# Kernel optimization log

Measured on AMD Instinct MI355X. Metric: run time of the kernel, lower is better.

The kernel has to match this reference:

```python
import jax, jax.numpy as jnp
import numpy as np

N_NODES = 50000
N_EDGES = 800000
IN_DIM = 128
OUT_DIM = 128
NUM_RELS = 8


def setup_inputs() -> dict:
    key = jax.random.key(0)
    k_feat, k_rel, k_w, k_src, k_dst, k_rt = jax.random.split(key, 6)
    feat = jax.random.normal(k_feat, (N_NODES, IN_DIM), dtype=jnp.float32)
    # xavier_uniform over (in_dim, out_dim) fan
    limit = float(np.sqrt(6.0 / (IN_DIM + OUT_DIM)))
    rel_emb = jax.random.uniform(k_rel, (NUM_RELS, IN_DIM, OUT_DIM), dtype=jnp.float32,
                                 minval=-limit, maxval=limit)
    edge_weight = jax.random.uniform(k_w, (N_EDGES,), dtype=jnp.float32)
    src = jax.random.randint(k_src, (N_EDGES,), 0, N_NODES, dtype=jnp.int32)
    dst = jax.random.randint(k_dst, (N_EDGES,), 0, N_NODES, dtype=jnp.int32)
    rel_type = jax.random.randint(k_rt, (N_EDGES,), 0, NUM_RELS, dtype=jnp.int32)
    return {"feat": feat, "rel_emb": rel_emb, "edge_weight": edge_weight,
            "src": src, "dst": dst, "rel_type": rel_type}


def reference(feat, rel_emb, edge_weight, src, dst, rel_type):
    # src_feat: [E, in] gather of source-node features
    src_feat = feat[src]
    num_rels = rel_emb.shape[0]
    # Equivalent to bmm(src_feat[:,None,:], rel_emb[rel_type]).squeeze(1)
    # but avoids materializing the [E, in, out] per-edge weight tensor:
    # loop over the small fixed relation set with masked accumulation.
    msg = jnp.zeros((src_feat.shape[0], rel_emb.shape[2]), dtype=src_feat.dtype)
    for r in range(num_rels):
        mask = (rel_type == r)[:, None]
        msg = msg + jnp.where(mask, src_feat @ rel_emb[r], jnp.zeros((), dtype=src_feat.dtype))
    msg = msg * edge_weight[:, None]
    # copy_e + sum aggregation onto destination nodes: [N, out]
    return jax.ops.segment_sum(msg, dst, num_segments=feat.shape[0])
```

## Files before the change

kernel.cpp:

```cpp
#include <hip/hip_runtime.h>
#include <stdint.h>

#define N_NODES   50000
#define N_EDGES   800000
#define IN_DIM    128
#define OUT_DIM   128
#define NUM_RELS  8
#define THREADS   256

typedef _Float16 half_t;
typedef _Float16 half2v __attribute__((ext_vector_type(2)));
typedef _Float16 half4v __attribute__((ext_vector_type(4)));
typedef _Float16 half8 __attribute__((ext_vector_type(8)));
typedef float floatx4 __attribute__((ext_vector_type(4)));


#define NBINS3    N_NODES
#define NB3       ((NBINS3 + 1023) / 1024)

#define WS_Y2     0
#define WS_OFF    102400000
#define WS_WT     102600064
#define WS_BASE   102862208
#define WS_WGT    106062208
#define WS_HIST   107662208
#define WS_BSUM   107862208
#define WS_NEED   (size_t)107862464

__global__ void prep_hist_kernel(const float* __restrict__ rel_emb, half_t* __restrict__ WT,
                                 const int* __restrict__ dst, int* __restrict__ hist) {
    int b = blockIdx.x;
    if (b < 512) {
        int t = b * 256 + threadIdx.x;
        int r = t >> 14, k = (t >> 7) & 127, n = t & 127;
        WT[(size_t)((r << 7) | n) * 128 + k] = (half_t)rel_emb[t];
    } else {
        int i = (b - 512) * 256 + threadIdx.x;
        if (i < N_EDGES) atomicAdd(&hist[dst[i]], 1);
    }
}

__global__ void scan1_kernel(const int* __restrict__ hist, int* __restrict__ bsum) {
    __shared__ int sh[256];
    int b = blockIdx.x, t = threadIdx.x;
    int i0 = b * 1024 + t * 4;
    int s = 0;
    #pragma unroll
    for (int j = 0; j < 4; j++) { int idx = i0 + j; if (idx < NBINS3) s += hist[idx]; }
    sh[t] = s; __syncthreads();
    for (int o = 128; o > 0; o >>= 1) { if (t < o) sh[t] += sh[t + o]; __syncthreads(); }
    if (t == 0) bsum[b] = sh[0];
}

__global__ void scan2_kernel(int* __restrict__ bsum, int* __restrict__ off) {
    __shared__ int sh[64];
    int t = threadIdx.x;
    int v = (t < NB3) ? bsum[t] : 0;
    sh[t] = v; __syncthreads();
    for (int o = 1; o < 64; o <<= 1) {
        int x = (t >= o) ? sh[t - o] : 0;
        __syncthreads();
        sh[t] += x;
        __syncthreads();
    }
    if (t < NB3) bsum[t] = sh[t] - v;
    if (t == 0) off[NBINS3] = N_EDGES;
}

__global__ void scan3_kernel(const int* __restrict__ hist, const int* __restrict__ boff,
                             int* __restrict__ off, int* __restrict__ cursors) {
    __shared__ int sh[256];
    int b = blockIdx.x, t = threadIdx.x;
    int i0 = b * 1024 + t * 4;
    int v[4]; int s = 0;
    #pragma unroll
    for (int j = 0; j < 4; j++) { int idx = i0 + j; v[j] = (idx < NBINS3) ? hist[idx] : 0; s += v[j]; }
    sh[t] = s; __syncthreads();
    for (int o = 1; o < 256; o <<= 1) {
        int x = (t >= o) ? sh[t - o] : 0;
        __syncthreads();
        sh[t] += x;
        __syncthreads();
    }
    int run = sh[t] - s + boff[b];
    #pragma unroll
    for (int j = 0; j < 4; j++) {
        int idx = i0 + j;
        if (idx < NBINS3) { off[idx] = run; cursors[idx] = run; }
        run += v[j];
    }
}

__global__ void scatter3_kernel(const int* __restrict__ dst, const int* __restrict__ src,
                                const int* __restrict__ rel, const float* __restrict__ ew,
                                int* __restrict__ cursors, int* __restrict__ base,
                                half_t* __restrict__ wgt) {
    int i = blockIdx.x * blockDim.x + threadIdx.x;
    if (i < N_EDGES) {
        int pos = atomicAdd(&cursors[dst[i]], 1);
        base[pos] = src[i] * 1024 + rel[i] * 128;
        wgt[pos] = (half_t)ew[i];
    }
}

template<bool GUARD>
__device__ __forceinline__ void gemm_body(const float* __restrict__ feat,
                                          half_t* __restrict__ Ws,
                                          half_t* __restrict__ y2,
                                          int m0, int n0, int wave, int lane) {
    const int q = lane >> 4, l16 = lane & 15;
    const int wm0 = m0 + wave * 32;

    float4 fr[2][4][2];
    #pragma unroll
    for (int ms = 0; ms < 2; ms++) {
        int node = wm0 + ms * 16 + l16;
        const float* fb = feat + (size_t)node * 128 + q * 8;
        bool ok = !GUARD || node < N_NODES;
        #pragma unroll
        for (int kk = 0; kk < 4; kk++)
            #pragma unroll
            for (int h = 0; h < 2; h++) {
                float4 v = {0.f, 0.f, 0.f, 0.f};
                if (ok) v = *(const float4*)(fb + kk * 32 + h * 4);
                fr[ms][kk][h] = v;
            }
    }
    __syncthreads();

    half8 bf[2][4];
    #pragma unroll
    for (int ms = 0; ms < 2; ms++)
        #pragma unroll
        for (int kk = 0; kk < 4; kk++) {
            half8 hb;
            hb[0] = (half_t)fr[ms][kk][0].x; hb[1] = (half_t)fr[ms][kk][0].y;
            hb[2] = (half_t)fr[ms][kk][0].z; hb[3] = (half_t)fr[ms][kk][0].w;
            hb[4] = (half_t)fr[ms][kk][1].x; hb[5] = (half_t)fr[ms][kk][1].y;
            hb[6] = (half_t)fr[ms][kk][1].z; hb[7] = (half_t)fr[ms][kk][1].w;
            bf[ms][kk] = hb;
        }

    floatx4 acc[8][2];
    #pragma unroll
    for (int nt = 0; nt < 8; nt++)
        #pragma unroll
        for (int ms = 0; ms < 2; ms++) acc[nt][ms] = (floatx4){0.f, 0.f, 0.f, 0.f};

    #pragma unroll
    for (int kk = 0; kk < 4; kk++) {
        #pragma unroll
        for (int nt = 0; nt < 8; nt++) {
            int row = nt * 16 + l16;
            int phys = (kk * 4 + q) ^ (l16 & 7);
            half8 a = *(const half8*)(Ws + row * 128 + phys * 8);
            acc[nt][0] = __builtin_amdgcn_mfma_f32_16x16x32_f16(a, bf[0][kk], acc[nt][0], 0, 0, 0);
            acc[nt][1] = __builtin_amdgcn_mfma_f32_16x16x32_f16(a, bf[1][kk], acc[nt][1], 0, 0, 0);
        }
    }

    __syncthreads();

    #pragma unroll
    for (int nt = 0; nt < 8; nt++)
        #pragma unroll
        for (int ms = 0; ms < 2; ms++) {
            int nl = wave * 32 + ms * 16 + l16;
            int c  = nt * 4 + q;
            int p  = (c + nl) & 31;
            half4v hv;
            hv[0] = (half_t)acc[nt][ms][0]; hv[1] = (half_t)acc[nt][ms][1];
            hv[2] = (half_t)acc[nt][ms][2]; hv[3] = (half_t)acc[nt][ms][3];
            *(half4v*)(Ws + nl * 128 + p * 4) = hv;
        }
    #pragma unroll
    for (int i = 0; i < 8; i++) {
        int nl  = wave * 32 + i * 4 + (lane >> 4);
        int c16 = lane & 15;
        int p0 = (2 * c16 + nl) & 31;
        int p1 = (2 * c16 + 1 + nl) & 31;
        uint2 lo = *(const uint2*)(Ws + nl * 128 + p0 * 4);
        uint2 hi = *(const uint2*)(Ws + nl * 128 + p1 * 4);
        int node = m0 + nl;
        if (!GUARD || node < N_NODES) {
            uint4 v; v.x = lo.x; v.y = lo.y; v.z = hi.x; v.w = hi.y;
            *(uint4*)(y2 + (size_t)node * 1024 + n0 + c16 * 8) = v;
        }
    }
}

#define GY_GRID (391 * 8)
__global__ __launch_bounds__(THREADS) void gemm_y_kernel(
    const float* __restrict__ feat, const half_t* __restrict__ WT,
    half_t* __restrict__ y2) {
    __shared__ half_t Ws[128 * 128];
    int bid = blockIdx.x;
    int work = (bid & 7) * 391 + (bid >> 3);
    int mt = work >> 3, nt8 = work & 7;
    const int m0 = mt * 128, n0 = nt8 * 128;
    const int t = threadIdx.x;
    const int wave = t >> 6, lane = t & 63;

    for (int i = t; i < 2048; i += THREADS) {
        int row = i >> 4, lc = i & 15;
        int phys = lc ^ (row & 7);
        *(uint4*)&Ws[row * 128 + phys * 8] =
            *(const uint4*)(WT + (size_t)(n0 + row) * 128 + lc * 8);
    }
    if (m0 + 128 <= N_NODES)
        gemm_body<false>(feat, Ws, y2, m0, n0, wave, lane);
    else
        gemm_body<true>(feat, Ws, y2, m0, n0, wave, lane);
}

__global__ __launch_bounds__(THREADS) void gather_kernel(
    const half_t* __restrict__ y2, const int* __restrict__ base,
    const half_t* __restrict__ wgt, const int* __restrict__ off,
    float* __restrict__ out) {
    int g = blockIdx.x * 4 + (threadIdx.x >> 6);
    int lane = threadIdx.x & 63;
    int beg = off[g], end = off[g + 1];
    const half_t* yb = y2 + lane * 2;
    float ax = 0.f, ay = 0.f, cx = 0.f, cy = 0.f;
    int e = beg;
    for (; e + 8 <= end; e += 8) {
        int b0 = base[e], b1 = base[e + 1], b2 = base[e + 2], b3 = base[e + 3];
        int b4 = base[e + 4], b5 = base[e + 5], b6 = base[e + 6], b7 = base[e + 7];
        half2v v0 = *(const half2v*)(yb + b0);
        half2v v1 = *(const half2v*)(yb + b1);
        half2v v2 = *(const half2v*)(yb + b2);
        half2v v3 = *(const half2v*)(yb + b3);
        half2v v4 = *(const half2v*)(yb + b4);
        half2v v5 = *(const half2v*)(yb + b5);
        half2v v6 = *(const half2v*)(yb + b6);
        half2v v7 = *(const half2v*)(yb + b7);
        float w0 = (float)wgt[e],     w1 = (float)wgt[e + 1];
        float w2 = (float)wgt[e + 2], w3 = (float)wgt[e + 3];
        float w4 = (float)wgt[e + 4], w5 = (float)wgt[e + 5];
        float w6 = (float)wgt[e + 6], w7 = (float)wgt[e + 7];
        ax += w0 * (float)v0[0] + w1 * (float)v1[0];
        ay += w0 * (float)v0[1] + w1 * (float)v1[1];
        cx += w2 * (float)v2[0] + w3 * (float)v3[0];
        cy += w2 * (float)v2[1] + w3 * (float)v3[1];
        ax += w4 * (float)v4[0] + w5 * (float)v5[0];
        ay += w4 * (float)v4[1] + w5 * (float)v5[1];
        cx += w6 * (float)v6[0] + w7 * (float)v7[0];
        cy += w6 * (float)v6[1] + w7 * (float)v7[1];
    }
    for (; e + 2 <= end; e += 2) {
        int b0 = base[e], b1 = base[e + 1];
        float w0 = (float)wgt[e], w1 = (float)wgt[e + 1];
        half2v v0 = *(const half2v*)(yb + b0);
        half2v v1 = *(const half2v*)(yb + b1);
        ax += w0 * (float)v0[0] + w1 * (float)v1[0];
        ay += w0 * (float)v0[1] + w1 * (float)v1[1];
    }
    if (e < end) {
        int b0 = base[e];
        float w0 = (float)wgt[e];
        half2v v0 = *(const half2v*)(yb + b0);
        cx += w0 * (float)v0[0];
        cy += w0 * (float)v0[1];
    }
    float2 o; o.x = ax + cx; o.y = ay + cy;
    *(float2*)(out + (size_t)g * 128 + lane * 2) = o;
}

__global__ void naive_kernel(const float* __restrict__ feat, const float* __restrict__ rel_emb,
                             const float* __restrict__ ew, const int* __restrict__ src,
                             const int* __restrict__ dst, const int* __restrict__ rel,
                             float* __restrict__ out) {
    int wave = (blockIdx.x * blockDim.x + threadIdx.x) >> 6;
    int lane = threadIdx.x & 63;
    if (wave >= N_EDGES) return;
    const float* f = feat + (size_t)src[wave] * IN_DIM;
    const float* W = rel_emb + (size_t)rel[wave] * IN_DIM * OUT_DIM;
    float w = ew[wave];
    float a0 = 0.f, a1 = 0.f;
    for (int k = 0; k < IN_DIM; k++) {
        float fv = f[k];
        a0 += fv * W[k * OUT_DIM + lane];
        a1 += fv * W[k * OUT_DIM + 64 + lane];
    }
    int d = dst[wave];
    atomicAdd(&out[(size_t)d * OUT_DIM + lane], a0 * w);
    atomicAdd(&out[(size_t)d * OUT_DIM + 64 + lane], a1 * w);
}

extern "C" void kernel_launch(void* const* d_in, const int* in_sizes, int n_in,
                              void* d_out, int out_size, void* d_ws, size_t ws_size,
                              hipStream_t stream) {
    const float* feat    = (const float*)d_in[0];
    const float* rel_emb = (const float*)d_in[1];
    const float* ew      = (const float*)d_in[2];
    const int*   src     = (const int*)d_in[3];
    const int*   dst     = (const int*)d_in[4];
    const int*   rel     = (const int*)d_in[5];
    float* out = (float*)d_out;

    const int eb = (N_EDGES + THREADS - 1) / THREADS;

    if (ws_size >= WS_NEED) {
        char* ws = (char*)d_ws;
        half_t* y2    = (half_t*)(ws + WS_Y2);
        int*    off   = (int*)(ws + WS_OFF);
        half_t* WT    = (half_t*)(ws + WS_WT);
        int*    basep = (int*)(ws + WS_BASE);
        half_t* wgt   = (half_t*)(ws + WS_WGT);
        int*    hist  = (int*)(ws + WS_HIST);
        int*    bsum  = (int*)(ws + WS_BSUM);

        hipMemsetAsync(hist, 0, (size_t)NBINS3 * 4, stream);
        prep_hist_kernel<<<512 + eb, THREADS, 0, stream>>>(rel_emb, WT, dst, hist);
        gemm_y_kernel<<<GY_GRID, THREADS, 0, stream>>>(feat, WT, y2);
        scan1_kernel<<<NB3, 256, 0, stream>>>(hist, bsum);
        scan2_kernel<<<1, 64, 0, stream>>>(bsum, off);
        scan3_kernel<<<NB3, 256, 0, stream>>>(hist, bsum, off, hist);
        scatter3_kernel<<<eb, THREADS, 0, stream>>>(dst, src, rel, ew, hist, basep, wgt);
        gather_kernel<<<N_NODES / 4, THREADS, 0, stream>>>(y2, basep, wgt, off, out);
    } else {
        hipMemsetAsync(d_out, 0, (size_t)out_size * sizeof(float), stream);
        const long long total = (long long)N_EDGES * 64;
        const int blocks = (int)((total + THREADS - 1) / THREADS);
        naive_kernel<<<blocks, THREADS, 0, stream>>>(feat, rel_emb, ew, src, dst, rel, out);
    }
}
```

Measured before the change: 257.3 us.

## Fuse GEMM and edge scatter into one interleaved kernel; halve histogram blocks

Merges the per-relation GEMM kernel and the CSR scatter kernel into a single launch. Block groups alternate between GEMM tiles and scatter work, so the compute-bound GEMM overlaps with the atomic-heavy scatter, and the scans now run before both. The histogram part of the prep kernel also handles two edges per thread, halving its block count. The cost is that blocks in the fused kernel become heterogeneous: scatter blocks still reserve the GEMM's 32 KB of shared memory, which can limit occupancy.

```diff
diff --git a/kernel.cpp b/kernel.cpp
--- a/kernel.cpp
+++ b/kernel.cpp
@@ -27,6 +27,7 @@
 #define WS_BSUM   107862208
 #define WS_NEED   (size_t)107862464
 
+#define HIST_BLOCKS ((N_EDGES + 511) / 512)
 __global__ void prep_hist_kernel(const float* __restrict__ rel_emb, half_t* __restrict__ WT,
                                  const int* __restrict__ dst, int* __restrict__ hist) {
     int b = blockIdx.x;
@@ -35,8 +36,11 @@
         int r = t >> 14, k = (t >> 7) & 127, n = t & 127;
         WT[(size_t)((r << 7) | n) * 128 + k] = (half_t)rel_emb[t];
     } else {
-        int i = (b - 512) * 256 + threadIdx.x;
-        if (i < N_EDGES) atomicAdd(&hist[dst[i]], 1);
+        int i = (b - 512) * 512 + threadIdx.x;
+        int d0 = (i < N_EDGES) ? dst[i] : -1;
+        int d1 = (i + 256 < N_EDGES) ? dst[i + 256] : -1;
+        if (d0 >= 0) atomicAdd(&hist[d0], 1);
+        if (d1 >= 0) atomicAdd(&hist[d1], 1);
     }
 }
 
@@ -91,18 +95,6 @@
     }
 }
 
-__global__ void scatter3_kernel(const int* __restrict__ dst, const int* __restrict__ src,
-                                const int* __restrict__ rel, const float* __restrict__ ew,
-                                int* __restrict__ cursors, int* __restrict__ base,
-                                half_t* __restrict__ wgt) {
-    int i = blockIdx.x * blockDim.x + threadIdx.x;
-    if (i < N_EDGES) {
-        int pos = atomicAdd(&cursors[dst[i]], 1);
-        base[pos] = src[i] * 1024 + rel[i] * 128;
-        wgt[pos] = (half_t)ew[i];
-    }
-}
-
 template<bool GUARD>
 __device__ __forceinline__ void gemm_body(const float* __restrict__ feat,
                                           half_t* __restrict__ Ws,
@@ -160,7 +152,6 @@
     }
 
     __syncthreads();
-
     #pragma unroll
     for (int nt = 0; nt < 8; nt++)
         #pragma unroll
@@ -189,28 +180,41 @@
     }
 }
 
-#define GY_GRID (391 * 8)
-__global__ __launch_bounds__(THREADS) void gemm_y_kernel(
+#define FUSE_BLOCKS 6256
+__global__ __launch_bounds__(THREADS) void fused_kernel(
     const float* __restrict__ feat, const half_t* __restrict__ WT,
-    half_t* __restrict__ y2) {
+    half_t* __restrict__ y2,
+    const int* __restrict__ dst, const int* __restrict__ src,
+    const int* __restrict__ rel, const float* __restrict__ ew,
+    int* __restrict__ cursors, int* __restrict__ base, half_t* __restrict__ wgt) {
     __shared__ half_t Ws[128 * 128];
-    int bid = blockIdx.x;
-    int work = (bid & 7) * 391 + (bid >> 3);
-    int mt = work >> 3, nt8 = work & 7;
-    const int m0 = mt * 128, n0 = nt8 * 128;
+    const int bid = blockIdx.x;
     const int t = threadIdx.x;
-    const int wave = t >> 6, lane = t & 63;
-
-    for (int i = t; i < 2048; i += THREADS) {
-        int row = i >> 4, lc = i & 15;
-        int phys = lc ^ (row & 7);
-        *(uint4*)&Ws[row * 128 + phys * 8] =
-            *(const uint4*)(WT + (size_t)(n0 + row) * 128 + lc * 8);
-    }
-    if (m0 + 128 <= N_NODES)
-        gemm_body<false>(feat, Ws, y2, m0, n0, wave, lane);
-    else
-        gemm_body<true>(feat, Ws, y2, m0, n0, wave, lane);
+
+    if (((bid >> 3) & 1) == 0) {
+        int work = (bid & 7) * 391 + (bid >> 4);
+        int mt = work >> 3, nt8 = work & 7;
+        const int m0 = mt * 128, n0 = nt8 * 128;
+        const int wave = t >> 6, lane = t & 63;
+
+        for (int i = t; i < 2048; i += THREADS) {
+            int row = i >> 4, lc = i & 15;
+            int phys = lc ^ (row & 7);
+            *(uint4*)&Ws[row * 128 + phys * 8] =
+                *(const uint4*)(WT + (size_t)(n0 + row) * 128 + lc * 8);
+        }
+        if (m0 + 128 <= N_NODES)
+            gemm_body<false>(feat, Ws, y2, m0, n0, wave, lane);
+        else
+            gemm_body<true>(feat, Ws, y2, m0, n0, wave, lane);
+    } else {
+        int sblock = (bid >> 4) * 8 + (bid & 7);
+        if (sblock >= 3125) return;
+        int i = sblock * 256 + t;
+        int pos = atomicAdd(&cursors[dst[i]], 1);
+        base[pos] = src[i] * 1024 + rel[i] * 128;
+        wgt[pos] = (half_t)ew[i];
+    }
 }
 
 __global__ __launch_bounds__(THREADS) void gather_kernel(
@@ -298,8 +302,6 @@
     const int*   rel     = (const int*)d_in[5];
     float* out = (float*)d_out;
 
-    const int eb = (N_EDGES + THREADS - 1) / THREADS;
-
     if (ws_size >= WS_NEED) {
         char* ws = (char*)d_ws;
         half_t* y2    = (half_t*)(ws + WS_Y2);
@@ -311,12 +313,12 @@
         int*    bsum  = (int*)(ws + WS_BSUM);
 
         hipMemsetAsync(hist, 0, (size_t)NBINS3 * 4, stream);
-        prep_hist_kernel<<<512 + eb, THREADS, 0, stream>>>(rel_emb, WT, dst, hist);
-        gemm_y_kernel<<<GY_GRID, THREADS, 0, stream>>>(feat, WT, y2);
+        prep_hist_kernel<<<512 + HIST_BLOCKS, THREADS, 0, stream>>>(rel_emb, WT, dst, hist);
         scan1_kernel<<<NB3, 256, 0, stream>>>(hist, bsum);
         scan2_kernel<<<1, 64, 0, stream>>>(bsum, off);
         scan3_kernel<<<NB3, 256, 0, stream>>>(hist, bsum, off, hist);
-        scatter3_kernel<<<eb, THREADS, 0, stream>>>(dst, src, rel, ew, hist, basep, wgt);
+        fused_kernel<<<FUSE_BLOCKS, THREADS, 0, stream>>>(feat, WT, y2, dst, src, rel, ew,
+                                                          hist, basep, wgt);
         gather_kernel<<<N_NODES / 4, THREADS, 0, stream>>>(y2, basep, wgt, off, out);
     } else {
         hipMemsetAsync(d_out, 0, (size_t)out_size * sizeof(float), stream);
```

Measured after the change: 255.4 us. Within noise of the previous version (-0.7%).
